# Optimization experiments

Hardware: AMD Instinct MI355X
Metric: run time of the kernel (lower is better)

The kernel has to match this reference:

```python
import jax, jax.numpy as jnp
import numpy as np

# Constants from init_kwargs
DT = 0.01
NIV = 8          # energy_input_dim[1]
HID = 64         # hidden_dims[0]
FEAT = 501       # per-field microstructure feature length (501+501=1002)


def _lin(k, fin, fout):
    return jax.random.normal(k, (fin, fout), dtype=jnp.float32) / np.sqrt(fin)


def setup_inputs() -> dict:
    key = jax.random.key(0)
    ks = jax.random.split(key, 12)
    B, T = 8192, 512
    e = jax.random.normal(ks[0], (B, T, 1), dtype=jnp.float32) * 0.1
    e_dot = jax.random.normal(ks[1], (B, T, 1), dtype=jnp.float32) * 0.1
    # positive microstructure fields (code computes nu**-1 and E/nu**2)
    E = jax.random.uniform(ks[2], (B, FEAT), minval=0.5, maxval=2.0, dtype=jnp.float32)
    nu = jax.random.uniform(ks[3], (B, FEAT), minval=0.5, maxval=2.0, dtype=jnp.float32)
    return {
        "e": e, "e_dot": e_dot, "E": E, "nu": nu,
        # EnergyFunction.B : Linear(1002,64) -> ReLU -> Linear(64,niv)
        "Bw1": _lin(ks[4], 2 * FEAT, HID), "Bb1": jnp.zeros((HID,), jnp.float32),
        "Bw2": _lin(ks[5], HID, NIV), "Bb2": jnp.zeros((NIV,), jnp.float32),
        # InverseDissipationPotential.beta : Linear(1002,64)->Softplus->Linear(64,niv)->Softplus
        "bw1": _lin(ks[6], 2 * FEAT, HID), "bb1": jnp.zeros((HID,), jnp.float32),
        "bw2": _lin(ks[7], HID, NIV), "bb2": jnp.zeros((NIV,), jnp.float32),
    }


def reference(e, e_dot, E, nu, Bw1, Bb1, Bw2, Bb2, bw1, bb1, bw2, bb2):
    # --- microstructure encoder (TrueFeatures) ---
    nu_p = 1.0 / jnp.mean(1.0 / nu, axis=1, keepdims=True)                 # [B,1]
    E_p = jnp.mean(E / nu ** 2, axis=1, keepdims=True) * nu_p ** 2         # [B,1]
    m = jnp.concatenate([E, nu], axis=-1)                                  # [B,1002]

    # Time-invariant MLP coefficients (hoisted out of the time loop)
    Bm = jax.nn.relu(m @ Bw1 + Bb1) @ Bw2 + Bb2                            # [B,NIV]
    beta = jax.nn.softplus(jax.nn.softplus(m @ bw1 + bb1) @ bw2 + bb2)     # [B,NIV]
    Bsum = jnp.sum(Bm, axis=-1, keepdims=True)                             # [B,1]

    B_, niv = Bm.shape
    xi0 = jnp.zeros((B_, niv), dtype=e.dtype)

    def step(xi, inp):
        u, p = inp                                                          # [B,1],[B,1]
        # Analytic gradients of L = sum_{b,k} Bm_bk * (0.5*E' u^2 + 0.5*(u-xi_k)^2 + 0.5*sum_j xi_j^2)
        du = u - xi                                                         # [B,NIV]
        grad_u = Bsum * E_p * u + jnp.sum(Bm * du, axis=-1, keepdims=True)  # [B,1] (s_eq)
        grad_v = -Bm * du + Bsum * xi                                       # [B,NIV] (d)
        q = -grad_v
        # Analytic gradients of potential = -0.5*nu' p^2 + 0.5*sum(beta*q^2)
        grad_p = -nu_p * p                                                  # [B,1] (s_neq)
        grad_q = beta * q                                                   # [B,NIV] (kinetics)
        stress = grad_u - grad_p
        return xi + DT * grad_q, (stress, xi)

    xs = (jnp.swapaxes(e, 0, 1), jnp.swapaxes(e_dot, 0, 1))                 # [T,B,1]
    _, (stress_t, xi_t) = jax.lax.scan(step, xi0, xs)
    stress = jnp.swapaxes(stress_t, 0, 1)                                   # [B,T,1]
    xi = jnp.swapaxes(xi_t, 0, 1)                                           # [B,T,NIV]
    return stress, xi
```

## Files before the change

kernel.cpp:

```cpp
#include <hip/hip_runtime.h>
#include <hip/hip_bf16.h>

#define FEATN 501
#define KPAD 1024
#define MSTRIDE 1032
#define NB 8192
#define NT 512
#define DTC 0.01f

typedef __attribute__((ext_vector_type(8))) short short8;
typedef __attribute__((ext_vector_type(4))) float f32x4;

__device__ __forceinline__ float softplus_f(float x) {
    return fmaxf(x, 0.f) + log1pf(expf(-fabsf(x)));
}
__device__ __forceinline__ ushort f2bf(float x) {
    __hip_bfloat16 h = __float2bfloat16(x);
    return *reinterpret_cast<ushort*>(&h);
}
__device__ __forceinline__ void gl_lds16(const void* g, void* l) {
    __builtin_amdgcn_global_load_lds(
        (const __attribute__((address_space(1))) void*)g,
        (__attribute__((address_space(3))) void*)l, 16, 0, 0);
}
__device__ __forceinline__ float dpp_add(float x, const int ctrl) {
    int s = __builtin_bit_cast(int, x);
    int y;
    switch (ctrl) {
    case 0xB1:  y = __builtin_amdgcn_update_dpp(0, s, 0xB1, 0xf, 0xf, true); break;
    case 0x4E:  y = __builtin_amdgcn_update_dpp(0, s, 0x4E, 0xf, 0xf, true); break;
    default:    y = __builtin_amdgcn_update_dpp(0, s, 0x141, 0xf, 0xf, true); break;
    }
    return x + __builtin_bit_cast(float, y);
}

__global__ __launch_bounds__(256) void wtrans_kernel(
    const float* __restrict__ Bw1, const float* __restrict__ bw1,
    ushort* __restrict__ Wt) {
    const int h = blockIdx.x;
    const float* W = (h < 64) ? Bw1 : bw1;
    const int col = h & 63;
    #pragma unroll
    for (int it = 0; it < 4; ++it) {
        const int k = it * 256 + threadIdx.x;
        const int ksrc = (k < FEATN) ? k
                       : (k >= 512 && k < 512 + FEATN) ? k - 11 : -1;
        const float v = (ksrc >= 0) ? W[(size_t)ksrc * 64 + col] : 0.f;
        Wt[(size_t)(((k >> 5) * 128 + h) * 4 + ((k >> 3) & 3)) * 8 + (k & 7)] =
            f2bf(v);
    }
}

__global__ __launch_bounds__(1024, 8) void enc_kernel(
    const float* __restrict__ E, const float* __restrict__ nu,
    const ushort* __restrict__ Wt,
    const float* __restrict__ Bb1, const float* __restrict__ bb1,
    const float* __restrict__ Bw2, const float* __restrict__ Bb2,
    const float* __restrict__ bw2, const float* __restrict__ bb2,
    float* __restrict__ cw) {
    __shared__ ushort Ml[16 * MSTRIDE];
    __shared__ float red[3][2048];
    __shared__ float hid[128][17];
    __shared__ float nups[16], Eps[16];

    const int tid = threadIdx.x;
    const int w = tid >> 6, lane = tid & 63;
    const int bb0 = blockIdx.x * 16;

    {
        const size_t base = (size_t)(bb0 + w) * FEATN;
        float s1 = 0.f, s2 = 0.f;
        for (int i = lane; i < FEATN; i += 64) {
            const float Ev = E[base + i];
            const float nv = nu[base + i];
            const float inv = 1.0f / nv;
            s1 += inv;
            s2 = fmaf(Ev, inv * inv, s2);
            Ml[w * MSTRIDE + i] = f2bf(Ev);
            Ml[w * MSTRIDE + 512 + i] = f2bf(nv);
        }
        if (lane < 11) {
            Ml[w * MSTRIDE + FEATN + lane] = 0;
            Ml[w * MSTRIDE + 512 + FEATN + lane] = 0;
        }
        #pragma unroll
        for (int o = 32; o; o >>= 1) {
            s1 += __shfl_xor(s1, o);
            s2 += __shfl_xor(s2, o);
        }
        if (lane == 0) {
            const float np = (float)FEATN / s1;
            nups[w] = np;
            Eps[w] = (s2 / (float)FEATN) * np * np;
        }
    }
    __syncthreads();

    const int g = w & 3, q = w >> 2;
    const int r15 = lane & 15, kg = lane >> 4;
    {
        const ushort* wbase = Wt + (size_t)(q * 8) * 4096;
        const int aoff = (g * 32 + r15) * 32 + kg * 8;
        const int boff = r15 * MSTRIDE + q * 256 + kg * 8;

        f32x4 acc0 = {0.f, 0.f, 0.f, 0.f}, acc1 = acc0;
        #pragma unroll
        for (int s = 0; s < 8; ++s) {
            const short8 a0 = *(const short8*)(wbase + s * 4096 + aoff);
            const short8 a1 = *(const short8*)(wbase + s * 4096 + aoff + 512);
            const short8 b = *(const short8*)&Ml[boff + s * 32];
            acc0 = __builtin_amdgcn_mfma_f32_16x16x32_bf16(a0, b, acc0, 0, 0, 0);
            acc1 = __builtin_amdgcn_mfma_f32_16x16x32_bf16(a1, b, acc1, 0, 0, 0);
        }
        if (q > 0) {
            *(f32x4*)&red[q - 1][(g * 64 + lane) * 8] = acc0;
            *(f32x4*)&red[q - 1][(g * 64 + lane) * 8 + 4] = acc1;
        }
        __syncthreads();
        if (q == 0) {
            #pragma unroll
            for (int p = 0; p < 3; ++p) {
                acc0 += *(const f32x4*)&red[p][(g * 64 + lane) * 8];
                acc1 += *(const f32x4*)&red[p][(g * 64 + lane) * 8 + 4];
            }
            #pragma unroll
            for (int t = 0; t < 2; ++t) {
                #pragma unroll
                for (int r = 0; r < 4; ++r) {
                    const int h = g * 32 + t * 16 + kg * 4 + r;
                    const float bias = (h < 64) ? Bb1[h] : bb1[h - 64];
                    float v = (t ? acc1[r] : acc0[r]) + bias;
                    v = (h < 64) ? fmaxf(v, 0.f) : softplus_f(v);
                    hid[h][r15] = v;
                }
            }
        }
    }
    __syncthreads();

    if (tid < 128) {
        const int bl = tid >> 3, k = tid & 7;
        float dB = 0.f, db = 0.f;
        #pragma unroll 8
        for (int h = 0; h < 64; ++h) {
            dB = fmaf(hid[h][bl], Bw2[h * 8 + k], dB);
            db = fmaf(hid[64 + h][bl], bw2[h * 8 + k], db);
        }
        const float Bm = dB + Bb2[k];
        const float be = softplus_f(db + bb2[k]);
        float Bs = Bm;
        Bs += __shfl_xor(Bs, 1);
        Bs += __shfl_xor(Bs, 2);
        Bs += __shfl_xor(Bs, 4);
        float* cb = cw + (size_t)(bb0 + bl) * 32;
        cb[k] = 1.f - DTC * be * (Bm + Bs);
        cb[8 + k] = DTC * be * Bm;
        cb[16 + k] = Bm;
        if (k == 0) {
            cb[24] = Bs * (Eps[bl] + 1.f);
            cb[25] = nups[bl];
        }
    }
}

__global__ __launch_bounds__(256) void time_kernel(
    const float* __restrict__ e, const float* __restrict__ ed,
    const float* __restrict__ cw, float* __restrict__ stress,
    float* __restrict__ xi_out) {
    __shared__ float els[4][512];
    __shared__ float pls[4][512];
    const int wv = threadIdx.x >> 6;
    const int wid = (blockIdx.x << 2) + wv;
    const int lane = threadIdx.x & 63;
    const int j = lane >> 3, k = lane & 7;

    const float* eb = e + (size_t)wid * NT;
    const float* edb = ed + (size_t)wid * NT;
    gl_lds16(eb + lane * 4, &els[wv][0]);
    gl_lds16(eb + 256 + lane * 4, &els[wv][256]);
    gl_lds16(edb + lane * 4, &pls[wv][0]);
    gl_lds16(edb + 256 + lane * 4, &pls[wv][256]);

    const float* cb = cw + (size_t)wid * 32;
    const float a = cb[k];
    const float c = cb[8 + k];
    const float Bm = cb[16 + k];
    const float sE2 = cb[24];
    const float nup = cb[25];
    asm volatile("s_waitcnt vmcnt(0)" ::: "memory");

    const float a2 = a * a, a4 = a2 * a2;
    float A = 1.f;
    if (j & 1) A *= a;
    if (j & 2) A *= a2;
    if (j & 4) A *= a4;
    float pw[8];
    {
        float run = c;
        #pragma unroll
        for (int i = 7; i >= 0; --i) {
            const bool on = (i < j);
            pw[i] = on ? run : 0.f;
            run = on ? run * a : run;
        }
    }

    float* xb = xi_out + (size_t)wid * (NT * 8);
    float* sb = stress + (size_t)wid * NT;
    const float* el = &els[wv][0];
    const float* pl = &pls[wv][0];

    float xs = 0.f;
    #pragma unroll
    for (int it = 0; it < 64; ++it) {
        const int t0 = it * 8;
        const float4 q0 = *(const float4*)(el + t0);
        const float4 q1 = *(const float4*)(el + t0 + 4);
        const float cuj = el[t0 + j];
        const float cpj = pl[t0 + j];
        float xi_j = A * xs;
        xi_j = fmaf(pw[0], q0.x, xi_j);
        xi_j = fmaf(pw[1], q0.y, xi_j);
        xi_j = fmaf(pw[2], q0.z, xi_j);
        xi_j = fmaf(pw[3], q0.w, xi_j);
        xi_j = fmaf(pw[4], q1.x, xi_j);
        xi_j = fmaf(pw[5], q1.y, xi_j);
        xi_j = fmaf(pw[6], q1.z, xi_j);
        xi_j = fmaf(pw[7], q1.w, xi_j);
        xb[t0 * 8 + lane] = xi_j;
        float r = Bm * xi_j;
        r = dpp_add(r, 0xB1);
        r = dpp_add(r, 0x4E);
        r = dpp_add(r, 0x141);
        if (k == 0)
            sb[t0 + j] = fmaf(cuj, sE2, fmaf(nup, cpj, -r));
        xs = fmaf(a, __shfl(xi_j, 56 + k), c * q1.w);
    }
}

extern "C" void kernel_launch(void* const* d_in, const int* in_sizes, int n_in,
                              void* d_out, int out_size, void* d_ws, size_t ws_size,
                              hipStream_t stream) {
    const float* e   = (const float*)d_in[0];
    const float* ed  = (const float*)d_in[1];
    const float* E   = (const float*)d_in[2];
    const float* nu  = (const float*)d_in[3];
    const float* Bw1 = (const float*)d_in[4];
    const float* Bb1 = (const float*)d_in[5];
    const float* Bw2 = (const float*)d_in[6];
    const float* Bb2 = (const float*)d_in[7];
    const float* bw1 = (const float*)d_in[8];
    const float* bb1 = (const float*)d_in[9];
    const float* bw2 = (const float*)d_in[10];
    const float* bb2 = (const float*)d_in[11];

    float* out = (float*)d_out;
    float* stress = out;
    float* xi = out + (size_t)NB * NT;
    ushort* Wt = (ushort*)d_ws;
    float* cw = (float*)((char*)d_ws + (1 << 20));

    wtrans_kernel<<<128, 256, 0, stream>>>(Bw1, bw1, Wt);
    enc_kernel<<<512, 1024, 0, stream>>>(E, nu, Wt, Bb1, bb1,
                                         Bw2, Bb2, bw2, bb2, cw);
    time_kernel<<<2048, 256, 0, stream>>>(e, ed, cw, stress, xi);
}
```

Measured before the change: 60.64 us.

## Restructure encoder to 8 batch rows per 256-thread block without split-K reduction

The encoder kernel now processes 8 batch rows per 256-thread block instead of 16 rows per 1024-thread block. Each wave covers the full K dimension in 32 MFMA steps, which removes the cross-wave split-K reduction through shared memory and one barrier. The cost is that half of each MFMA's B columns are duplicated and wasted (only 8 real rows in a 16-wide tile). Each wave also does a longer serial K loop, though the grid doubles, which helps occupancy and scheduling.

```diff
diff --git a/kernel.cpp b/kernel.cpp
--- a/kernel.cpp
+++ b/kernel.cpp
@@ -51,24 +51,25 @@
     }
 }
 
-__global__ __launch_bounds__(1024, 8) void enc_kernel(
+__global__ __launch_bounds__(256, 8) void enc_kernel(
     const float* __restrict__ E, const float* __restrict__ nu,
     const ushort* __restrict__ Wt,
     const float* __restrict__ Bb1, const float* __restrict__ bb1,
     const float* __restrict__ Bw2, const float* __restrict__ Bb2,
     const float* __restrict__ bw2, const float* __restrict__ bb2,
     float* __restrict__ cw) {
-    __shared__ ushort Ml[16 * MSTRIDE];
-    __shared__ float red[3][2048];
-    __shared__ float hid[128][17];
-    __shared__ float nups[16], Eps[16];
+    __shared__ ushort Ml[8 * MSTRIDE];
+    __shared__ float hid[128][9];
+    __shared__ float nups[8], Eps[8];
 
     const int tid = threadIdx.x;
     const int w = tid >> 6, lane = tid & 63;
-    const int bb0 = blockIdx.x * 16;
-
-    {
-        const size_t base = (size_t)(bb0 + w) * FEATN;
+    const int bb0 = blockIdx.x * 8;
+
+    #pragma unroll
+    for (int bp = 0; bp < 2; ++bp) {
+        const int bl = w * 2 + bp;
+        const size_t base = (size_t)(bb0 + bl) * FEATN;
         float s1 = 0.f, s2 = 0.f;
         for (int i = lane; i < FEATN; i += 64) {
             const float Ev = E[base + i];
@@ -76,12 +77,12 @@
             const float inv = 1.0f / nv;
             s1 += inv;
             s2 = fmaf(Ev, inv * inv, s2);
-            Ml[w * MSTRIDE + i] = f2bf(Ev);
-            Ml[w * MSTRIDE + 512 + i] = f2bf(nv);
+            Ml[bl * MSTRIDE + i] = f2bf(Ev);
+            Ml[bl * MSTRIDE + 512 + i] = f2bf(nv);
         }
         if (lane < 11) {
-            Ml[w * MSTRIDE + FEATN + lane] = 0;
-            Ml[w * MSTRIDE + 512 + FEATN + lane] = 0;
+            Ml[bl * MSTRIDE + FEATN + lane] = 0;
+            Ml[bl * MSTRIDE + 512 + FEATN + lane] = 0;
         }
         #pragma unroll
         for (int o = 32; o; o >>= 1) {
@@ -90,44 +91,32 @@
         }
         if (lane == 0) {
             const float np = (float)FEATN / s1;
-            nups[w] = np;
-            Eps[w] = (s2 / (float)FEATN) * np * np;
+            nups[bl] = np;
+            Eps[bl] = (s2 / (float)FEATN) * np * np;
         }
     }
     __syncthreads();
 
-    const int g = w & 3, q = w >> 2;
     const int r15 = lane & 15, kg = lane >> 4;
     {
-        const ushort* wbase = Wt + (size_t)(q * 8) * 4096;
-        const int aoff = (g * 32 + r15) * 32 + kg * 8;
-        const int boff = r15 * MSTRIDE + q * 256 + kg * 8;
+        const ushort* wp = Wt + (size_t)(w * 32 + r15) * 32 + kg * 8;
+        const int boff = (r15 & 7) * MSTRIDE + kg * 8;
 
         f32x4 acc0 = {0.f, 0.f, 0.f, 0.f}, acc1 = acc0;
-        #pragma unroll
-        for (int s = 0; s < 8; ++s) {
-            const short8 a0 = *(const short8*)(wbase + s * 4096 + aoff);
-            const short8 a1 = *(const short8*)(wbase + s * 4096 + aoff + 512);
+        #pragma unroll 4
+        for (int s = 0; s < 32; ++s) {
+            const short8 a0 = *(const short8*)(wp + (size_t)s * 4096);
+            const short8 a1 = *(const short8*)(wp + (size_t)s * 4096 + 512);
             const short8 b = *(const short8*)&Ml[boff + s * 32];
             acc0 = __builtin_amdgcn_mfma_f32_16x16x32_bf16(a0, b, acc0, 0, 0, 0);
             acc1 = __builtin_amdgcn_mfma_f32_16x16x32_bf16(a1, b, acc1, 0, 0, 0);
         }
-        if (q > 0) {
-            *(f32x4*)&red[q - 1][(g * 64 + lane) * 8] = acc0;
-            *(f32x4*)&red[q - 1][(g * 64 + lane) * 8 + 4] = acc1;
-        }
-        __syncthreads();
-        if (q == 0) {
-            #pragma unroll
-            for (int p = 0; p < 3; ++p) {
-                acc0 += *(const f32x4*)&red[p][(g * 64 + lane) * 8];
-                acc1 += *(const f32x4*)&red[p][(g * 64 + lane) * 8 + 4];
-            }
+        if (r15 < 8) {
             #pragma unroll
             for (int t = 0; t < 2; ++t) {
                 #pragma unroll
                 for (int r = 0; r < 4; ++r) {
-                    const int h = g * 32 + t * 16 + kg * 4 + r;
+                    const int h = w * 32 + t * 16 + kg * 4 + r;
                     const float bias = (h < 64) ? Bb1[h] : bb1[h - 64];
                     float v = (t ? acc1[r] : acc0[r]) + bias;
                     v = (h < 64) ? fmaxf(v, 0.f) : softplus_f(v);
@@ -138,7 +127,7 @@
     }
     __syncthreads();
 
-    if (tid < 128) {
+    if (tid < 64) {
         const int bl = tid >> 3, k = tid & 7;
         float dB = 0.f, db = 0.f;
         #pragma unroll 8
@@ -261,7 +250,7 @@
     float* cw = (float*)((char*)d_ws + (1 << 20));
 
     wtrans_kernel<<<128, 256, 0, stream>>>(Bw1, bw1, Wt);
-    enc_kernel<<<512, 1024, 0, stream>>>(E, nu, Wt, Bb1, bb1,
+    enc_kernel<<<1024, 256, 0, stream>>>(E, nu, Wt, Bb1, bb1,
                                          Bw2, Bb2, bw2, bb2, cw);
     time_kernel<<<2048, 256, 0, stream>>>(e, ed, cw, stress, xi);
 }
```

After: 69.29 us. 1.14x slower.

## Keep encoder weights in registers and process two row groups per block

Applied to the files above, without the earlier changes.

The encoder kernel now loads its bf16 first-layer weight fragments into registers once and reuses them across two 16-row batch groups, halving the grid. E and nu rows are staged into LDS with direct global-to-LDS loads. The split-K reduction, bias and activation are spread across all threads, and the second-layer weights and biases are cached in shared memory. The second-layer dot product is split across lanes and combined with shuffles. The cost is much more shared memory per block (a 64KB raw staging buffer plus a larger reduction array), which limits occupancy. The extra barriers also serialise the two groups inside each block.

```diff
diff --git a/kernel.cpp b/kernel.cpp
--- a/kernel.cpp
+++ b/kernel.cpp
@@ -2,11 +2,11 @@
 #include <hip/hip_bf16.h>
 
 #define FEATN 501
-#define KPAD 1024
 #define MSTRIDE 1032
 #define NB 8192
 #define NT 512
 #define DTC 0.01f
+#define RAWS 1024
 
 typedef __attribute__((ext_vector_type(8))) short short8;
 typedef __attribute__((ext_vector_type(4))) float f32x4;
@@ -51,114 +51,140 @@
     }
 }
 
-__global__ __launch_bounds__(1024, 8) void enc_kernel(
+__global__ __launch_bounds__(1024) void enc_kernel(
     const float* __restrict__ E, const float* __restrict__ nu,
     const ushort* __restrict__ Wt,
     const float* __restrict__ Bb1, const float* __restrict__ bb1,
     const float* __restrict__ Bw2, const float* __restrict__ Bb2,
     const float* __restrict__ bw2, const float* __restrict__ bb2,
     float* __restrict__ cw) {
+    __shared__ float raw[16 * RAWS];
     __shared__ ushort Ml[16 * MSTRIDE];
-    __shared__ float red[3][2048];
+    __shared__ float red[4][2048];
     __shared__ float hid[128][17];
+    __shared__ float w2B[512], w2b[512];
+    __shared__ float b1s[128], b2s[16];
     __shared__ float nups[16], Eps[16];
 
     const int tid = threadIdx.x;
     const int w = tid >> 6, lane = tid & 63;
-    const int bb0 = blockIdx.x * 16;
-
-    {
-        const size_t base = (size_t)(bb0 + w) * FEATN;
-        float s1 = 0.f, s2 = 0.f;
-        for (int i = lane; i < FEATN; i += 64) {
-            const float Ev = E[base + i];
-            const float nv = nu[base + i];
-            const float inv = 1.0f / nv;
-            s1 += inv;
-            s2 = fmaf(Ev, inv * inv, s2);
-            Ml[w * MSTRIDE + i] = f2bf(Ev);
-            Ml[w * MSTRIDE + 512 + i] = f2bf(nv);
-        }
-        if (lane < 11) {
-            Ml[w * MSTRIDE + FEATN + lane] = 0;
-            Ml[w * MSTRIDE + 512 + FEATN + lane] = 0;
-        }
-        #pragma unroll
-        for (int o = 32; o; o >>= 1) {
-            s1 += __shfl_xor(s1, o);
-            s2 += __shfl_xor(s2, o);
-        }
-        if (lane == 0) {
-            const float np = (float)FEATN / s1;
-            nups[w] = np;
-            Eps[w] = (s2 / (float)FEATN) * np * np;
-        }
-    }
-    __syncthreads();
-
     const int g = w & 3, q = w >> 2;
     const int r15 = lane & 15, kg = lane >> 4;
+    const int bb0 = blockIdx.x * 32;
+    const size_t NTOT = (size_t)NB * FEATN;
+
+    if (tid < 512) { w2B[tid] = Bw2[tid]; w2b[tid] = bw2[tid]; }
+    else if (tid < 576) { b1s[tid - 512] = Bb1[tid - 512]; }
+    else if (tid < 640) { b1s[128 - 640 + tid] = bb1[tid - 576]; }
+    else if (tid < 648) { b2s[tid - 640] = Bb2[tid - 640]; }
+    else if (tid < 656) { b2s[8 + tid - 648] = bb2[tid - 648]; }
+
+    short8 wa[8], wb[8];
     {
-        const ushort* wbase = Wt + (size_t)(q * 8) * 4096;
-        const int aoff = (g * 32 + r15) * 32 + kg * 8;
-        const int boff = r15 * MSTRIDE + q * 256 + kg * 8;
-
-        f32x4 acc0 = {0.f, 0.f, 0.f, 0.f}, acc1 = acc0;
+        const ushort* wp = Wt + (size_t)(q * 8) * 4096 + (g * 32 + r15) * 32 + kg * 8;
         #pragma unroll
         for (int s = 0; s < 8; ++s) {
-            const short8 a0 = *(const short8*)(wbase + s * 4096 + aoff);
-            const short8 a1 = *(const short8*)(wbase + s * 4096 + aoff + 512);
-            const short8 b = *(const short8*)&Ml[boff + s * 32];
-            acc0 = __builtin_amdgcn_mfma_f32_16x16x32_bf16(a0, b, acc0, 0, 0, 0);
-            acc1 = __builtin_amdgcn_mfma_f32_16x16x32_bf16(a1, b, acc1, 0, 0, 0);
-        }
-        if (q > 0) {
-            *(f32x4*)&red[q - 1][(g * 64 + lane) * 8] = acc0;
-            *(f32x4*)&red[q - 1][(g * 64 + lane) * 8 + 4] = acc1;
+            wa[s] = *(const short8*)(wp + s * 4096);
+            wb[s] = *(const short8*)(wp + s * 4096 + 512);
+        }
+    }
+
+    for (int g2 = 0; g2 < 2; ++g2) {
+        const int b = bb0 + g2 * 16 + w;
+        if (g2) __syncthreads();
+
+        {
+            const size_t bidx = (size_t)b * FEATN;
+            size_t al = bidx & ~(size_t)3;
+            if (al + 512 > NTOT) al = NTOT - 512;
+            const int dlt = (int)(bidx - al);
+            float* rw = &raw[w * RAWS];
+            gl_lds16(E + al + lane * 4, rw);
+            gl_lds16(E + al + 256 + lane * 4, rw + 256);
+            gl_lds16(nu + al + lane * 4, rw + 512);
+            gl_lds16(nu + al + 256 + lane * 4, rw + 768);
+            asm volatile("s_waitcnt vmcnt(0)" ::: "memory");
+
+            float s1 = 0.f, s2 = 0.f;
+            for (int i = lane; i < FEATN; i += 64) {
+                const float Ev = rw[dlt + i];
+                const float nv = rw[512 + dlt + i];
+                const float inv = 1.0f / nv;
+                s1 += inv;
+                s2 = fmaf(Ev, inv * inv, s2);
+                Ml[w * MSTRIDE + i] = f2bf(Ev);
+                Ml[w * MSTRIDE + 512 + i] = f2bf(nv);
+            }
+            if (lane < 11) {
+                Ml[w * MSTRIDE + FEATN + lane] = 0;
+                Ml[w * MSTRIDE + 512 + FEATN + lane] = 0;
+            }
+            #pragma unroll
+            for (int o = 32; o; o >>= 1) {
+                s1 += __shfl_xor(s1, o);
+                s2 += __shfl_xor(s2, o);
+            }
+            if (lane == 0) {
+                const float np = (float)FEATN / s1;
+                nups[w] = np;
+                Eps[w] = (s2 / (float)FEATN) * np * np;
+            }
         }
         __syncthreads();
-        if (q == 0) {
+
+        {
+            f32x4 acc0 = {0.f, 0.f, 0.f, 0.f}, acc1 = acc0;
+            const int boff = r15 * MSTRIDE + q * 256 + kg * 8;
             #pragma unroll
-            for (int p = 0; p < 3; ++p) {
-                acc0 += *(const f32x4*)&red[p][(g * 64 + lane) * 8];
-                acc1 += *(const f32x4*)&red[p][(g * 64 + lane) * 8 + 4];
-            }
+            for (int s = 0; s < 8; ++s) {
+                const short8 bf = *(const short8*)&Ml[boff + s * 32];
+                acc0 = __builtin_amdgcn_mfma_f32_16x16x32_bf16(wa[s], bf, acc0, 0, 0, 0);
+                acc1 = __builtin_amdgcn_mfma_f32_16x16x32_bf16(wb[s], bf, acc1, 0, 0, 0);
+            }
+            *(f32x4*)&red[q][g * 512 + lane * 8] = acc0;
+            *(f32x4*)&red[q][g * 512 + lane * 8 + 4] = acc1;
+        }
+        __syncthreads();
+
+        #pragma unroll
+        for (int v2 = 0; v2 < 2; ++v2) {
+            const int c = tid * 2 + v2;
+            float vv = red[0][c] + red[1][c] + red[2][c] + red[3][c];
+            const int gg = c >> 9, rem = c & 511;
+            const int ln = rem >> 3, tr = rem & 7;
+            const int h = gg * 32 + (tr >> 2) * 16 + (ln >> 4) * 4 + (tr & 3);
+            const int bl = ln & 15;
+            vv += b1s[h];
+            vv = (h < 64) ? fmaxf(vv, 0.f) : softplus_f(vv);
+            hid[h][bl] = vv;
+        }
+        __syncthreads();
+
+        {
+            const int kk = lane >> 3, hc = lane & 7;
+            float dB = 0.f, db = 0.f;
             #pragma unroll
-            for (int t = 0; t < 2; ++t) {
-                #pragma unroll
-                for (int r = 0; r < 4; ++r) {
-                    const int h = g * 32 + t * 16 + kg * 4 + r;
-                    const float bias = (h < 64) ? Bb1[h] : bb1[h - 64];
-                    float v = (t ? acc1[r] : acc0[r]) + bias;
-                    v = (h < 64) ? fmaxf(v, 0.f) : softplus_f(v);
-                    hid[h][r15] = v;
+            for (int i = 0; i < 8; ++i) {
+                const int h = hc * 8 + i;
+                dB = fmaf(hid[h][w], w2B[h * 8 + kk], dB);
+                db = fmaf(hid[64 + h][w], w2b[h * 8 + kk], db);
+            }
+            dB += __shfl_xor(dB, 1); dB += __shfl_xor(dB, 2); dB += __shfl_xor(dB, 4);
+            db += __shfl_xor(db, 1); db += __shfl_xor(db, 2); db += __shfl_xor(db, 4);
+            const float Bm = dB + b2s[kk];
+            const float be = softplus_f(db + b2s[8 + kk]);
+            float Bs = Bm;
+            Bs += __shfl_xor(Bs, 8); Bs += __shfl_xor(Bs, 16); Bs += __shfl_xor(Bs, 32);
+            if (hc == 0) {
+                float* cb = cw + (size_t)b * 32;
+                cb[kk] = 1.f - DTC * be * (Bm + Bs);
+                cb[8 + kk] = DTC * be * Bm;
+                cb[16 + kk] = Bm;
+                if (kk == 0) {
+                    cb[24] = Bs * (Eps[w] + 1.f);
+                    cb[25] = nups[w];
                 }
             }
-        }
-    }
-    __syncthreads();
-
-    if (tid < 128) {
-        const int bl = tid >> 3, k = tid & 7;
-        float dB = 0.f, db = 0.f;
-        #pragma unroll 8
-        for (int h = 0; h < 64; ++h) {
-            dB = fmaf(hid[h][bl], Bw2[h * 8 + k], dB);
-            db = fmaf(hid[64 + h][bl], bw2[h * 8 + k], db);
-        }
-        const float Bm = dB + Bb2[k];
-        const float be = softplus_f(db + bb2[k]);
-        float Bs = Bm;
-        Bs += __shfl_xor(Bs, 1);
-        Bs += __shfl_xor(Bs, 2);
-        Bs += __shfl_xor(Bs, 4);
-        float* cb = cw + (size_t)(bb0 + bl) * 32;
-        cb[k] = 1.f - DTC * be * (Bm + Bs);
-        cb[8 + k] = DTC * be * Bm;
-        cb[16 + k] = Bm;
-        if (k == 0) {
-            cb[24] = Bs * (Eps[bl] + 1.f);
-            cb[25] = nups[bl];
         }
     }
 }
@@ -261,7 +287,7 @@
     float* cw = (float*)((char*)d_ws + (1 << 20));
 
     wtrans_kernel<<<128, 256, 0, stream>>>(Bw1, bw1, Wt);
-    enc_kernel<<<512, 1024, 0, stream>>>(E, nu, Wt, Bb1, bb1,
+    enc_kernel<<<256, 1024, 0, stream>>>(E, nu, Wt, Bb1, bb1,
                                          Bw2, Bb2, bw2, bb2, cw);
     time_kernel<<<2048, 256, 0, stream>>>(e, ed, cw, stress, xi);
 }
```

New measurement: 65.29 us. +7.7%, slower.
